# Kernel optimization log

Measured on AMD Instinct MI355X. Metric: run time of the kernel, lower is better.

Reference implementation:

```python
import jax, jax.numpy as jnp
import numpy as np

D_MODEL = 1024
N_HEADS = 16
D_HEAD = D_MODEL // N_HEADS


def setup_inputs() -> dict:
    key = jax.random.key(0)
    k1, k2, k3, k4, k5, k6 = jax.random.split(key, 6)
    B, Q, T = 4, 1024, 4096
    s = 1.0 / np.sqrt(D_MODEL)  # ~ kaiming-uniform scale for Linear weights
    return {
        "q_in": jax.random.normal(k1, (B, Q, D_MODEL), dtype=jnp.float32),
        "kv_in": jax.random.normal(k2, (B, T, D_MODEL), dtype=jnp.float32),
        "Wq": jax.random.normal(k3, (D_MODEL, D_MODEL), dtype=jnp.float32) * s,
        "Wk": jax.random.normal(k4, (D_MODEL, D_MODEL), dtype=jnp.float32) * s,
        "Wv": jax.random.normal(k5, (D_MODEL, D_MODEL), dtype=jnp.float32) * s,
        "Wo": jax.random.normal(k6, (D_MODEL, D_MODEL), dtype=jnp.float32) * s,
    }


def reference(q_in, kv_in, Wq, Wk, Wv, Wo):
    B, Q, D = q_in.shape
    T = kv_in.shape[1]
    scale = D_HEAD ** -0.5
    # projections; torch Linear: y = x @ W.T
    q = (q_in @ Wq.T).reshape(B, Q, N_HEADS, D_HEAD)
    k = (kv_in @ Wk.T).reshape(B, T, N_HEADS, D_HEAD)
    v = (kv_in @ Wv.T).reshape(B, T, N_HEADS, D_HEAD)
    # scores [B, H, Q, T]
    w = jnp.einsum("bqhd,bthd->bhqt", q, k) * scale
    w = jax.nn.softmax(w.astype(jnp.float32), axis=-1).astype(q.dtype)
    # dropout p=0.0 -> identity
    out = jnp.einsum("bhqt,bthd->bqhd", w, v).reshape(B, Q, D)
    return out @ Wo.T
```

## Files before the change

### kernel.cpp

```cpp
#include <hip/hip_runtime.h>
#include <hip/hip_bf16.h>
#include <cstdint>
#include <cstddef>

#define DM 1024
#define NH 16
#define DH 64
#define BQ 1024
#define TT 4096
#define BB 4
#define NSPLIT 2
#define TSPLIT (TT / NSPLIT)

using f32x4 = __attribute__((ext_vector_type(4))) float;
using f32x16 = __attribute__((ext_vector_type(16))) float;
using s16x8 = __attribute__((ext_vector_type(8))) short;

__device__ __forceinline__ unsigned short f2bf(float f) {
  union { __hip_bfloat16 h; unsigned short u; } c;
  c.h = __float2bfloat16(f);
  return c.u;
}

__device__ __forceinline__ float exp2_raw(float x) {
  return __builtin_amdgcn_exp2f(x);
}

__device__ __forceinline__ f32x16 fill16(float v) {
  f32x16 z;
#pragma unroll
  for (int i = 0; i < 16; i++) z[i] = v;
  return z;
}

__device__ __forceinline__ int pack2(float lo, float hi2) {
  return (int)((unsigned int)f2bf(lo) | ((unsigned int)f2bf(hi2) << 16));
}

template<int RB>
__device__ __forceinline__ s16x8 mkfrag(const f32x16& p, int hi) {
  const int W1 = pack2(p[RB + 0], p[RB + 1]);
  const int W3 = pack2(p[RB + 2], p[RB + 3]);
  const int W2 = pack2(p[RB + 4], p[RB + 5]);
  const int W4 = pack2(p[RB + 6], p[RB + 7]);
  const int s1 = __shfl_xor(W1, 32);
  const int s3 = __shfl_xor(W3, 32);
  const int s2 = __shfl_xor(W2, 32);
  const int s4 = __shfl_xor(W4, 32);
  union { int i[4]; s16x8 v; } u;
  u.i[0] = hi ? s2 : W1;
  u.i[1] = hi ? s4 : W3;
  u.i[2] = hi ? W2 : s1;
  u.i[3] = hi ? W4 : s3;
  return u.v;
}

__global__ void cvt_f32_bf16(const float* __restrict__ in, unsigned short* __restrict__ out, int n4) {
  int i = blockIdx.x * blockDim.x + threadIdx.x;
  if (i < n4) {
    float4 v = reinterpret_cast<const float4*>(in)[i];
    ushort4 o;
    o.x = f2bf(v.x); o.y = f2bf(v.y); o.z = f2bf(v.z); o.w = f2bf(v.w);
    reinterpret_cast<ushort4*>(out)[i] = o;
  }
}

__global__ void cvt_w4(const float* __restrict__ w0, const float* __restrict__ w1,
                       const float* __restrict__ w2, const float* __restrict__ w3,
                       unsigned short* __restrict__ o0, unsigned short* __restrict__ o1,
                       unsigned short* __restrict__ o2, unsigned short* __restrict__ o3,
                       int n4) {
  int i = blockIdx.x * blockDim.x + threadIdx.x;
  if (i >= n4) return;
  const float* in; unsigned short* out;
  switch (blockIdx.y) {
    case 0: in = w0; out = o0; break;
    case 1: in = w1; out = o1; break;
    case 2: in = w2; out = o2; break;
    default: in = w3; out = o3; break;
  }
  float4 v = reinterpret_cast<const float4*>(in)[i];
  ushort4 o;
  o.x = f2bf(v.x); o.y = f2bf(v.y); o.z = f2bf(v.z); o.w = f2bf(v.w);
  reinterpret_cast<ushort4*>(out)[i] = o;
}

__device__ __forceinline__ void gload_lds16(const unsigned short* g, unsigned short* l) {
  __builtin_amdgcn_global_load_lds(
      (const __attribute__((address_space(1))) unsigned int*)g,
      (__attribute__((address_space(3))) unsigned int*)l,
      16, 0, 0);
}

__device__ __forceinline__ int xcd_swz(int lin, int nwg) {
  return (lin & 7) * (nwg >> 3) + (lin >> 3);
}


#define GEMM_STAGE(AS, BS, BUF)                                              \
  do {                                                                       \
    _Pragma("unroll")                                                        \
    for (int s = 0; s < 4; s++) {                                            \
      gload_lds16(gA + (size_t)(s * 8) * DM, &AS[BUF][(wid * 32 + s * 8) * 64]); \
      gload_lds16(gW + (size_t)(s * 8) * DM, &BS[BUF][(wid * 32 + s * 8) * 64]); \
    }                                                                        \
    gA += 64; gW += 64;                                                      \
  } while (0)

#define GEMM_COMPUTE(AS, BS, BUF)                                            \
  do {                                                                       \
    __builtin_amdgcn_s_setprio(1);                                           \
    _Pragma("unroll")                                                        \
    for (int kk = 0; kk < 2; kk++) {                                         \
      s16x8 af[4], bfv[4];                                                   \
      _Pragma("unroll")                                                      \
      for (int mt = 0; mt < 4; mt++) {                                       \
        const int row = wr * 64 + mt * 16 + fr;                              \
        af[mt] = *reinterpret_cast<const s16x8*>(                            \
            &AS[BUF][row * 64 + (((kk * 4 + fkg) ^ (fr & 7)) * 8)]);         \
      }                                                                      \
      _Pragma("unroll")                                                      \
      for (int nt = 0; nt < 4; nt++) {                                       \
        const int row = wc * 64 + nt * 16 + fr;                              \
        bfv[nt] = *reinterpret_cast<const s16x8*>(                           \
            &BS[BUF][row * 64 + (((kk * 4 + fkg) ^ (fr & 7)) * 8)]);         \
      }                                                                      \
      _Pragma("unroll")                                                      \
      for (int mt = 0; mt < 4; mt++)                                         \
        _Pragma("unroll")                                                    \
        for (int nt = 0; nt < 4; nt++)                                       \
          acc[mt][nt] = __builtin_amdgcn_mfma_f32_16x16x32_bf16(             \
              af[mt], bfv[nt], acc[mt][nt], 0, 0, 0);                        \
    }                                                                        \
    __builtin_amdgcn_s_setprio(0);                                           \
  } while (0)

template<int MODE, int SEQ, bool PRESCALE, int NT>
__global__ __launch_bounds__(256) void gemm_bt(const unsigned short* __restrict__ A,
                                               const unsigned short* __restrict__ W,
                                               unsigned short* __restrict__ Cb,
                                               float* __restrict__ Cf) {
  __shared__ unsigned short As[2][128 * 64];
  __shared__ unsigned short Bs[2][128 * 64];
  const int tid = threadIdx.x;
  const int wid = tid >> 6, lane = tid & 63;
  const int swz = xcd_swz(blockIdx.x, gridDim.x);
  const int m0 = (swz / NT) * 128, n0 = (swz % NT) * 128;
  const int wr = wid >> 1, wc = wid & 1;
  const int fr = lane & 15;
  const int fkg = lane >> 4;

  f32x4 acc[4][4];
#pragma unroll
  for (int mt = 0; mt < 4; mt++)
#pragma unroll
    for (int nt = 0; nt < 4; nt++) acc[mt][nt] = f32x4{0.f, 0.f, 0.f, 0.f};

  const int srow = lane >> 3;
  const int sc8 = (lane & 7) ^ (srow & 7);
  const unsigned short* gA = A + (size_t)(m0 + wid * 32 + srow) * DM + sc8 * 8;
  const unsigned short* gW = W + (size_t)(n0 + wid * 32 + srow) * DM + sc8 * 8;

  GEMM_STAGE(As, Bs, 0);
  __syncthreads();
  for (int kt = 0; kt < DM / 64; kt += 2) {
    if (kt + 1 < DM / 64) GEMM_STAGE(As, Bs, 1);
    GEMM_COMPUTE(As, Bs, 0);
    __syncthreads();
    if (kt + 2 < DM / 64) GEMM_STAGE(As, Bs, 0);
    GEMM_COMPUTE(As, Bs, 1);
    __syncthreads();
  }

#pragma unroll
  for (int mt = 0; mt < 4; mt++) {
#pragma unroll
    for (int nt = 0; nt < 4; nt++) {
      const int col = n0 + wc * 64 + nt * 16 + fr;
#pragma unroll
      for (int r = 0; r < 4; r++) {
        const int m = m0 + wr * 64 + mt * 16 + (lane >> 4) * 4 + r;
        float v = acc[mt][nt][r];
        if constexpr (PRESCALE) v *= 0.18033688011112042f;
        if constexpr (MODE == 0) {
          const int b = m / SEQ, sr = m % SEQ;
          const int h = col >> 6, dh = col & 63;
          Cb[((size_t)(b * NH + h) * SEQ + sr) * DH + dh] = f2bf(v);
        } else {
          Cf[(size_t)m * DM + col] = v;
        }
      }
    }
  }
}

__global__ __launch_bounds__(256) void gemm_kv(const unsigned short* __restrict__ A,
                                               const unsigned short* __restrict__ Wkv,
                                               unsigned short* __restrict__ Kp,
                                               unsigned short* __restrict__ Vt) {
  __shared__ unsigned short As[2][128 * 64];
  __shared__ unsigned short Bs[2][128 * 64];
  const int tid = threadIdx.x;
  const int wid = tid >> 6, lane = tid & 63;
  const int swz = xcd_swz(blockIdx.x, gridDim.x);
  const int m0 = (swz >> 4) * 128, n0 = (swz & 15) * 128;
  const int wr = wid >> 1, wc = wid & 1;
  const int fr = lane & 15;
  const int fkg = lane >> 4;

  f32x4 acc[4][4];
#pragma unroll
  for (int mt = 0; mt < 4; mt++)
#pragma unroll
    for (int nt = 0; nt < 4; nt++) acc[mt][nt] = f32x4{0.f, 0.f, 0.f, 0.f};

  const int srow = lane >> 3;
  const int sc8 = (lane & 7) ^ (srow & 7);
  const unsigned short* gA = A + (size_t)(m0 + wid * 32 + srow) * DM + sc8 * 8;
  const unsigned short* gW = Wkv + (size_t)(n0 + wid * 32 + srow) * DM + sc8 * 8;

  GEMM_STAGE(As, Bs, 0);
  __syncthreads();
  for (int kt = 0; kt < DM / 64; kt += 2) {
    if (kt + 1 < DM / 64) GEMM_STAGE(As, Bs, 1);
    GEMM_COMPUTE(As, Bs, 0);
    __syncthreads();
    if (kt + 2 < DM / 64) GEMM_STAGE(As, Bs, 0);
    GEMM_COMPUTE(As, Bs, 1);
    __syncthreads();
  }

  const int klg = lane >> 4;
#pragma unroll
  for (int mt = 0; mt < 4; mt++) {
#pragma unroll
    for (int nt = 0; nt < 4; nt++) {
      const int col = n0 + wc * 64 + nt * 16 + fr;
      const int tb = m0 + wr * 64 + mt * 16 + klg * 4;
      const int b = tb >> 12, sr = tb & (TT - 1);
      if (col < DM) {
        const int h = col >> 6, dh = col & 63;
#pragma unroll
        for (int r = 0; r < 4; r++)
          Kp[((size_t)(b * NH + h) * TT + sr + r) * DH + dh] = f2bf(acc[mt][nt][r]);
      } else {
        const int c2 = col - DM;
        const int h = c2 >> 6, dh = c2 & 63;
        ushort4 pk;
        pk.x = f2bf(acc[mt][nt][0]);
        pk.y = f2bf(acc[mt][nt][1]);
        pk.z = f2bf(acc[mt][nt][2]);
        pk.w = f2bf(acc[mt][nt][3]);
        *reinterpret_cast<ushort4*>(&Vt[((size_t)(b * NH + h) * DH + dh) * TT + sr]) = pk;
      }
    }
  }
}

#define ATTN_TILE(CUR, DO_STAGE, SBUF)                                             \
  do {                                                                             \
    if (DO_STAGE) {                                                                \
      gload_lds16(gK, &KVs[(SBUF)][wid * 512]);                                    \
      gload_lds16(gV, &KVs[2 + (SBUF)][wid * 512]);                                \
      gK += 64 * DH; gV += 64;                                                     \
    }                                                                              \
    f32x16 s0 = fill16(-7.0f), s1 = fill16(-7.0f);                                 \
    __builtin_amdgcn_s_setprio(1);                                                 \
    _Pragma("unroll")                                                              \
    for (int kk = 0; kk < 4; kk++) {                                               \
      s16x8 kb0 = *reinterpret_cast<const s16x8*>(lds0 + (CUR) * 8192 + offA[kk]); \
      s0 = __builtin_amdgcn_mfma_f32_32x32x16_bf16(kb0, qf[kk], s0, 0, 0, 0);      \
      s16x8 kb1 = *reinterpret_cast<const s16x8*>(lds0 + (CUR) * 8192 + offB[kk]); \
      s1 = __builtin_amdgcn_mfma_f32_32x32x16_bf16(kb1, qf[kk], s1, 0, 0, 0);      \
    }                                                                              \
    __builtin_amdgcn_s_setprio(0);                                                 \
    _Pragma("unroll")                                                              \
    for (int r = 0; r < 16; r++) {                                                 \
      s0[r] = exp2_raw(s0[r]); lsum += s0[r];                                      \
      s1[r] = exp2_raw(s1[r]); lsum += s1[r];                                      \
    }                                                                              \
    s16x8 pa[4];                                                                   \
    pa[0] = mkfrag<0>(s0, hi);                                                     \
    pa[1] = mkfrag<8>(s0, hi);                                                     \
    pa[2] = mkfrag<0>(s1, hi);                                                     \
    pa[3] = mkfrag<8>(s1, hi);                                                     \
    __builtin_amdgcn_s_setprio(1);                                                 \
    _Pragma("unroll")                                                              \
    for (int kk = 0; kk < 4; kk++) {                                               \
      s16x8 vb0 = *reinterpret_cast<const s16x8*>(lds0 + 16384 + (CUR) * 8192 + offA[kk]); \
      o0 = __builtin_amdgcn_mfma_f32_32x32x16_bf16(pa[kk], vb0, o0, 0, 0, 0);      \
      s16x8 vb1 = *reinterpret_cast<const s16x8*>(lds0 + 16384 + (CUR) * 8192 + offB[kk]); \
      o1 = __builtin_amdgcn_mfma_f32_32x32x16_bf16(pa[kk], vb1, o1, 0, 0, 0);      \
    }                                                                              \
    __builtin_amdgcn_s_setprio(0);                                                 \
    __syncthreads();                                                               \
  } while (0)

__global__ __launch_bounds__(512, 4) void attn_kern(const unsigned short* __restrict__ Qp,
                                                    const unsigned short* __restrict__ Kp,
                                                    const unsigned short* __restrict__ Vtg,
                                                    float* __restrict__ Opart,
                                                    float* __restrict__ lsums) {
  __shared__ unsigned short KVs[4][64 * 64];
  const int bh = blockIdx.x;
  const int q0 = blockIdx.y * 256;
  const int split = blockIdx.z;
  const int t00 = split * TSPLIT;
  const int tid = threadIdx.x, wid = tid >> 6, lane = tid & 63;
  const int l31 = lane & 31, hi = lane >> 5;

  const size_t qrow = (size_t)bh * BQ + q0 + wid * 32 + l31;
  s16x8 qf[4];
#pragma unroll
  for (int kk = 0; kk < 4; kk++)
    qf[kk] = *reinterpret_cast<const s16x8*>(&Qp[qrow * DH + 16 * kk + 8 * hi]);

  f32x16 o0 = fill16(0.f), o1 = fill16(0.f);
  float lsum = 0.f;

  const size_t kvbase = (size_t)bh * TT * DH;
  const int rk = tid >> 3;
  const int c8 = tid & 7;

  const unsigned short* gK = Kp + kvbase + (size_t)(t00 + rk) * DH + (c8 ^ (rk & 7)) * 8;
  const unsigned short* gV = Vtg + kvbase + (size_t)rk * TT + t00 + (c8 ^ (rk & 7)) * 8;

  const char* lds0 = (const char*)&KVs[0][0];
  const int sw = l31 & 7;
  int offA[4], offB[4];
#pragma unroll
  for (int kk = 0; kk < 4; kk++) {
    offA[kk] = (l31 * 64 + (((2 * kk + hi) ^ sw) * 8)) * 2;
    offB[kk] = ((32 + l31) * 64 + (((2 * kk + hi) ^ sw) * 8)) * 2;
  }

  gload_lds16(gK, &KVs[0][wid * 512]);
  gload_lds16(gV, &KVs[2][wid * 512]);
  gK += 64 * DH; gV += 64;
  __syncthreads();

  const int NIT = TSPLIT / 128;
  for (int it2 = 0; it2 < NIT; ++it2) {
    ATTN_TILE(0, true, 1);
    ATTN_TILE(1, (it2 < NIT - 1), 0);
  }

  lsum += __shfl_xor(lsum, 32);
  if (lane < 32)
    lsums[((size_t)split * (BB * NH) + bh) * BQ + q0 + wid * 32 + lane] = lsum;

#pragma unroll
  for (int r = 0; r < 16; r++) {
    const int q = (r & 3) + 8 * (r >> 2) + 4 * hi;
    const size_t orow = (((size_t)split * (BB * NH) + bh) * BQ + q0 + wid * 32 + q) * DH;
    Opart[orow + l31] = o0[r];
    Opart[orow + 32 + l31] = o1[r];
  }
}

__global__ __launch_bounds__(256) void attn_combine(const float* __restrict__ Opart,
                                                    const float* __restrict__ lsums,
                                                    unsigned short* __restrict__ Ob) {
  const int gid = blockIdx.x * 256 + threadIdx.x;
  const int row = gid >> 4, seg = gid & 15;
  float denom = 0.f;
#pragma unroll
  for (int s = 0; s < NSPLIT; s++) denom += lsums[(size_t)s * (BB * NH * BQ) + row];
  const float inv = 1.0f / denom;
  float4 acc = {0.f, 0.f, 0.f, 0.f};
#pragma unroll
  for (int s = 0; s < NSPLIT; s++) {
    const float4 p = reinterpret_cast<const float4*>(Opart)[(size_t)s * (BB * NH * BQ) * 16 + (size_t)row * 16 + seg];
    acc.x += p.x; acc.y += p.y; acc.z += p.z; acc.w += p.w;
  }
  const int bh = row >> 10, q = row & (BQ - 1);
  const int b = bh >> 4, h = bh & 15;
  ushort4 o;
  o.x = f2bf(acc.x * inv);
  o.y = f2bf(acc.y * inv);
  o.z = f2bf(acc.z * inv);
  o.w = f2bf(acc.w * inv);
  *reinterpret_cast<ushort4*>(&Ob[((size_t)b * BQ + q) * DM + h * DH + seg * 4]) = o;
}

extern "C" void kernel_launch(void* const* d_in, const int* in_sizes, int n_in,
                              void* d_out, int out_size, void* d_ws, size_t ws_size,
                              hipStream_t stream) {
  const float* q_in = (const float*)d_in[0];
  const float* kv_in = (const float*)d_in[1];
  const float* Wq = (const float*)d_in[2];
  const float* Wk = (const float*)d_in[3];
  const float* Wv = (const float*)d_in[4];
  const float* Wo = (const float*)d_in[5];
  float* out = (float*)d_out;

  char* ws = (char*)d_ws;
  unsigned short* qin_b = (unsigned short*)ws;  ws += (size_t)BB * BQ * DM * 2;
  unsigned short* kvin_b = (unsigned short*)ws; ws += (size_t)BB * TT * DM * 2;
  unsigned short* Wq_b = (unsigned short*)ws;   ws += (size_t)DM * DM * 2;
  unsigned short* Wk_b = (unsigned short*)ws;   ws += (size_t)DM * DM * 2;
  unsigned short* Wv_b = (unsigned short*)ws;   ws += (size_t)DM * DM * 2;
  unsigned short* Wo_b = (unsigned short*)ws;   ws += (size_t)DM * DM * 2;
  unsigned short* qp = (unsigned short*)ws;     ws += (size_t)BB * NH * BQ * DH * 2;
  unsigned short* kp = (unsigned short*)ws;     ws += (size_t)BB * NH * TT * DH * 2;
  unsigned short* vt = (unsigned short*)ws;     ws += (size_t)BB * NH * DH * TT * 2;
  unsigned short* ao = (unsigned short*)ws;     ws += (size_t)BB * BQ * DM * 2;
  float* Opart = (float*)ws;                    ws += (size_t)NSPLIT * BB * NH * BQ * DH * 4;
  float* lsums = (float*)ws;                    ws += (size_t)NSPLIT * BB * NH * BQ * 4;

  const int qn4 = BB * BQ * DM / 4;
  const int kvn4 = BB * TT * DM / 4;
  const int wn4 = DM * DM / 4;
  cvt_f32_bf16<<<(qn4 + 255) / 256, 256, 0, stream>>>(q_in, qin_b, qn4);
  cvt_f32_bf16<<<(kvn4 + 255) / 256, 256, 0, stream>>>(kv_in, kvin_b, kvn4);
  cvt_w4<<<dim3((wn4 + 255) / 256, 4), 256, 0, stream>>>(Wq, Wk, Wv, Wo,
                                                         Wq_b, Wk_b, Wv_b, Wo_b, wn4);

  dim3 blk(256);
  gemm_bt<0, BQ, true, 8><<<dim3(BB * BQ / 128 * 8), blk, 0, stream>>>(qin_b, Wq_b, qp, nullptr);
  gemm_kv<<<dim3(BB * TT / 128 * 16), blk, 0, stream>>>(kvin_b, Wk_b, kp, vt);

  attn_kern<<<dim3(BB * NH, BQ / 256, NSPLIT), dim3(512), 0, stream>>>(qp, kp, vt, Opart, lsums);
  attn_combine<<<dim3(BB * NH * BQ * 16 / 256), blk, 0, stream>>>(Opart, lsums, ao);

  gemm_bt<1, BQ, false, 8><<<dim3(BB * BQ / 128 * 8), blk, 0, stream>>>(ao, Wo_b, nullptr, out);
}
```

Baseline: 243.7 us.

## Merge conversion and projection launches, double KV tile depth in attention

Merges the three fp32-to-bf16 conversion kernels into one launch, and merges the Q and KV projection GEMMs into one launch of 2304 blocks that branch on block index. The attention kernel now stages two 64-row K/V tiles per buffer slot (LDS doubled to 8 slots) and syncs once per 128 keys instead of once per 64. This cuts launch count, tail effects and barrier overhead. The cost is larger LDS use per block, which may lower attention occupancy.

```diff
diff --git a/kernel.cpp b/kernel.cpp
--- a/kernel.cpp
+++ b/kernel.cpp
@@ -55,34 +55,41 @@
   return u.v;
 }
 
-__global__ void cvt_f32_bf16(const float* __restrict__ in, unsigned short* __restrict__ out, int n4) {
+__global__ void cvt_all(const float* __restrict__ q_in, const float* __restrict__ kv_in,
+                        const float* __restrict__ w0, const float* __restrict__ w1,
+                        const float* __restrict__ w2, const float* __restrict__ w3,
+                        unsigned short* __restrict__ qo, unsigned short* __restrict__ kvo,
+                        unsigned short* __restrict__ o0, unsigned short* __restrict__ o1,
+                        unsigned short* __restrict__ o2, unsigned short* __restrict__ o3) {
+  const int KVN4 = BB * TT * DM / 4;
+  const int QN4 = BB * BQ * DM / 4;
+  const int WN4 = DM * DM / 4;
   int i = blockIdx.x * blockDim.x + threadIdx.x;
-  if (i < n4) {
-    float4 v = reinterpret_cast<const float4*>(in)[i];
-    ushort4 o;
-    o.x = f2bf(v.x); o.y = f2bf(v.y); o.z = f2bf(v.z); o.w = f2bf(v.w);
-    reinterpret_cast<ushort4*>(out)[i] = o;
-  }
-}
-
-__global__ void cvt_w4(const float* __restrict__ w0, const float* __restrict__ w1,
-                       const float* __restrict__ w2, const float* __restrict__ w3,
-                       unsigned short* __restrict__ o0, unsigned short* __restrict__ o1,
-                       unsigned short* __restrict__ o2, unsigned short* __restrict__ o3,
-                       int n4) {
-  int i = blockIdx.x * blockDim.x + threadIdx.x;
-  if (i >= n4) return;
-  const float* in; unsigned short* out;
-  switch (blockIdx.y) {
-    case 0: in = w0; out = o0; break;
-    case 1: in = w1; out = o1; break;
-    case 2: in = w2; out = o2; break;
-    default: in = w3; out = o3; break;
-  }
-  float4 v = reinterpret_cast<const float4*>(in)[i];
+  const float* in;
+  unsigned short* out;
+  int idx;
+  if (i < KVN4) {
+    in = kv_in; out = kvo; idx = i;
+  } else {
+    i -= KVN4;
+    if (i < QN4) {
+      in = q_in; out = qo; idx = i;
+    } else {
+      i -= QN4;
+      const int t = i >> 18;
+      idx = i & (WN4 - 1);
+      switch (t) {
+        case 0: in = w0; out = o0; break;
+        case 1: in = w1; out = o1; break;
+        case 2: in = w2; out = o2; break;
+        default: in = w3; out = o3; break;
+      }
+    }
+  }
+  float4 v = reinterpret_cast<const float4*>(in)[idx];
   ushort4 o;
   o.x = f2bf(v.x); o.y = f2bf(v.y); o.z = f2bf(v.z); o.w = f2bf(v.w);
-  reinterpret_cast<ushort4*>(out)[i] = o;
+  reinterpret_cast<ushort4*>(out)[idx] = o;
 }
 
 __device__ __forceinline__ void gload_lds16(const unsigned short* g, unsigned short* l) {
@@ -135,10 +142,103 @@
     __builtin_amdgcn_s_setprio(0);                                           \
   } while (0)
 
-template<int MODE, int SEQ, bool PRESCALE, int NT>
+__global__ __launch_bounds__(256) void gemm_proj(const unsigned short* __restrict__ qA,
+                                                 const unsigned short* __restrict__ kvA,
+                                                 const unsigned short* __restrict__ Wqb,
+                                                 const unsigned short* __restrict__ Wkv,
+                                                 unsigned short* __restrict__ Qp,
+                                                 unsigned short* __restrict__ Kp,
+                                                 unsigned short* __restrict__ Vt) {
+  __shared__ unsigned short As[2][128 * 64];
+  __shared__ unsigned short Bs[2][128 * 64];
+  const int tid = threadIdx.x;
+  const int wid = tid >> 6, lane = tid & 63;
+  const int swz = xcd_swz(blockIdx.x, gridDim.x);
+  const bool isQ = swz >= 2048;
+  int m0, n0;
+  const unsigned short *Abase, *Wbase;
+  if (isQ) {
+    const int qi = swz - 2048;
+    m0 = (qi >> 3) * 128; n0 = (qi & 7) * 128;
+    Abase = qA; Wbase = Wqb;
+  } else {
+    m0 = (swz >> 4) * 128; n0 = (swz & 15) * 128;
+    Abase = kvA; Wbase = Wkv;
+  }
+  const int wr = wid >> 1, wc = wid & 1;
+  const int fr = lane & 15;
+  const int fkg = lane >> 4;
+
+  f32x4 acc[4][4];
+#pragma unroll
+  for (int mt = 0; mt < 4; mt++)
+#pragma unroll
+    for (int nt = 0; nt < 4; nt++) acc[mt][nt] = f32x4{0.f, 0.f, 0.f, 0.f};
+
+  const int srow = lane >> 3;
+  const int sc8 = (lane & 7) ^ (srow & 7);
+  const unsigned short* gA = Abase + (size_t)(m0 + wid * 32 + srow) * DM + sc8 * 8;
+  const unsigned short* gW = Wbase + (size_t)(n0 + wid * 32 + srow) * DM + sc8 * 8;
+
+  GEMM_STAGE(As, Bs, 0);
+  __syncthreads();
+  for (int kt = 0; kt < DM / 64; kt += 2) {
+    if (kt + 1 < DM / 64) GEMM_STAGE(As, Bs, 1);
+    GEMM_COMPUTE(As, Bs, 0);
+    __syncthreads();
+    if (kt + 2 < DM / 64) GEMM_STAGE(As, Bs, 0);
+    GEMM_COMPUTE(As, Bs, 1);
+    __syncthreads();
+  }
+
+  const int klg = lane >> 4;
+  if (isQ) {
+#pragma unroll
+    for (int mt = 0; mt < 4; mt++) {
+#pragma unroll
+      for (int nt = 0; nt < 4; nt++) {
+        const int col = n0 + wc * 64 + nt * 16 + fr;
+        const int h = col >> 6, dh = col & 63;
+#pragma unroll
+        for (int r = 0; r < 4; r++) {
+          const int m = m0 + wr * 64 + mt * 16 + klg * 4 + r;
+          const int b = m >> 10, sr = m & (BQ - 1);
+          Qp[((size_t)(b * NH + h) * BQ + sr) * DH + dh] =
+              f2bf(acc[mt][nt][r] * 0.18033688011112042f);
+        }
+      }
+    }
+  } else {
+#pragma unroll
+    for (int mt = 0; mt < 4; mt++) {
+#pragma unroll
+      for (int nt = 0; nt < 4; nt++) {
+        const int col = n0 + wc * 64 + nt * 16 + fr;
+        const int tb = m0 + wr * 64 + mt * 16 + klg * 4;
+        const int b = tb >> 12, sr = tb & (TT - 1);
+        if (col < DM) {
+          const int h = col >> 6, dh = col & 63;
+#pragma unroll
+          for (int r = 0; r < 4; r++)
+            Kp[((size_t)(b * NH + h) * TT + sr + r) * DH + dh] = f2bf(acc[mt][nt][r]);
+        } else {
+          const int c2 = col - DM;
+          const int h = c2 >> 6, dh = c2 & 63;
+          ushort4 pk;
+          pk.x = f2bf(acc[mt][nt][0]);
+          pk.y = f2bf(acc[mt][nt][1]);
+          pk.z = f2bf(acc[mt][nt][2]);
+          pk.w = f2bf(acc[mt][nt][3]);
+          *reinterpret_cast<ushort4*>(&Vt[((size_t)(b * NH + h) * DH + dh) * TT + sr]) = pk;
+        }
+      }
+    }
+  }
+}
+
+template<int NT>
 __global__ __launch_bounds__(256) void gemm_bt(const unsigned short* __restrict__ A,
                                                const unsigned short* __restrict__ W,
-                                               unsigned short* __restrict__ Cb,
                                                float* __restrict__ Cf) {
   __shared__ unsigned short As[2][128 * 64];
   __shared__ unsigned short Bs[2][128 * 64];
@@ -180,97 +280,31 @@
 #pragma unroll
       for (int r = 0; r < 4; r++) {
         const int m = m0 + wr * 64 + mt * 16 + (lane >> 4) * 4 + r;
-        float v = acc[mt][nt][r];
-        if constexpr (PRESCALE) v *= 0.18033688011112042f;
-        if constexpr (MODE == 0) {
-          const int b = m / SEQ, sr = m % SEQ;
-          const int h = col >> 6, dh = col & 63;
-          Cb[((size_t)(b * NH + h) * SEQ + sr) * DH + dh] = f2bf(v);
-        } else {
-          Cf[(size_t)m * DM + col] = v;
-        }
+        Cf[(size_t)m * DM + col] = acc[mt][nt][r];
       }
     }
   }
 }
 
-__global__ __launch_bounds__(256) void gemm_kv(const unsigned short* __restrict__ A,
-                                               const unsigned short* __restrict__ Wkv,
-                                               unsigned short* __restrict__ Kp,
-                                               unsigned short* __restrict__ Vt) {
-  __shared__ unsigned short As[2][128 * 64];
-  __shared__ unsigned short Bs[2][128 * 64];
-  const int tid = threadIdx.x;
-  const int wid = tid >> 6, lane = tid & 63;
-  const int swz = xcd_swz(blockIdx.x, gridDim.x);
-  const int m0 = (swz >> 4) * 128, n0 = (swz & 15) * 128;
-  const int wr = wid >> 1, wc = wid & 1;
-  const int fr = lane & 15;
-  const int fkg = lane >> 4;
-
-  f32x4 acc[4][4];
-#pragma unroll
-  for (int mt = 0; mt < 4; mt++)
-#pragma unroll
-    for (int nt = 0; nt < 4; nt++) acc[mt][nt] = f32x4{0.f, 0.f, 0.f, 0.f};
-
-  const int srow = lane >> 3;
-  const int sc8 = (lane & 7) ^ (srow & 7);
-  const unsigned short* gA = A + (size_t)(m0 + wid * 32 + srow) * DM + sc8 * 8;
-  const unsigned short* gW = Wkv + (size_t)(n0 + wid * 32 + srow) * DM + sc8 * 8;
-
-  GEMM_STAGE(As, Bs, 0);
-  __syncthreads();
-  for (int kt = 0; kt < DM / 64; kt += 2) {
-    if (kt + 1 < DM / 64) GEMM_STAGE(As, Bs, 1);
-    GEMM_COMPUTE(As, Bs, 0);
-    __syncthreads();
-    if (kt + 2 < DM / 64) GEMM_STAGE(As, Bs, 0);
-    GEMM_COMPUTE(As, Bs, 1);
-    __syncthreads();
-  }
-
-  const int klg = lane >> 4;
-#pragma unroll
-  for (int mt = 0; mt < 4; mt++) {
-#pragma unroll
-    for (int nt = 0; nt < 4; nt++) {
-      const int col = n0 + wc * 64 + nt * 16 + fr;
-      const int tb = m0 + wr * 64 + mt * 16 + klg * 4;
-      const int b = tb >> 12, sr = tb & (TT - 1);
-      if (col < DM) {
-        const int h = col >> 6, dh = col & 63;
-#pragma unroll
-        for (int r = 0; r < 4; r++)
-          Kp[((size_t)(b * NH + h) * TT + sr + r) * DH + dh] = f2bf(acc[mt][nt][r]);
-      } else {
-        const int c2 = col - DM;
-        const int h = c2 >> 6, dh = c2 & 63;
-        ushort4 pk;
-        pk.x = f2bf(acc[mt][nt][0]);
-        pk.y = f2bf(acc[mt][nt][1]);
-        pk.z = f2bf(acc[mt][nt][2]);
-        pk.w = f2bf(acc[mt][nt][3]);
-        *reinterpret_cast<ushort4*>(&Vt[((size_t)(b * NH + h) * DH + dh) * TT + sr]) = pk;
-      }
-    }
-  }
-}
-
-#define ATTN_TILE(CUR, DO_STAGE, SBUF)                                             \
+
+#define ATTN_STAGE(SP)                                                       \
+  do {                                                                       \
+    gload_lds16(gK, &KVs[(SP) * 2][wid * 512]);                              \
+    gload_lds16(gK + 64 * DH, &KVs[(SP) * 2 + 1][wid * 512]);                \
+    gload_lds16(gV, &KVs[4 + (SP) * 2][wid * 512]);                          \
+    gload_lds16(gV + 64, &KVs[4 + (SP) * 2 + 1][wid * 512]);                 \
+    gK += 128 * DH; gV += 128;                                               \
+  } while (0)
+
+#define ATTN_COMPUTE(SLOT)                                                         \
   do {                                                                             \
-    if (DO_STAGE) {                                                                \
-      gload_lds16(gK, &KVs[(SBUF)][wid * 512]);                                    \
-      gload_lds16(gV, &KVs[2 + (SBUF)][wid * 512]);                                \
-      gK += 64 * DH; gV += 64;                                                     \
-    }                                                                              \
     f32x16 s0 = fill16(-7.0f), s1 = fill16(-7.0f);                                 \
     __builtin_amdgcn_s_setprio(1);                                                 \
     _Pragma("unroll")                                                              \
     for (int kk = 0; kk < 4; kk++) {                                               \
-      s16x8 kb0 = *reinterpret_cast<const s16x8*>(lds0 + (CUR) * 8192 + offA[kk]); \
+      s16x8 kb0 = *reinterpret_cast<const s16x8*>(lds0 + (SLOT) * 8192 + offA[kk]); \
       s0 = __builtin_amdgcn_mfma_f32_32x32x16_bf16(kb0, qf[kk], s0, 0, 0, 0);      \
-      s16x8 kb1 = *reinterpret_cast<const s16x8*>(lds0 + (CUR) * 8192 + offB[kk]); \
+      s16x8 kb1 = *reinterpret_cast<const s16x8*>(lds0 + (SLOT) * 8192 + offB[kk]); \
       s1 = __builtin_amdgcn_mfma_f32_32x32x16_bf16(kb1, qf[kk], s1, 0, 0, 0);      \
     }                                                                              \
     __builtin_amdgcn_s_setprio(0);                                                 \
@@ -287,13 +321,12 @@
     __builtin_amdgcn_s_setprio(1);                                                 \
     _Pragma("unroll")                                                              \
     for (int kk = 0; kk < 4; kk++) {                                               \
-      s16x8 vb0 = *reinterpret_cast<const s16x8*>(lds0 + 16384 + (CUR) * 8192 + offA[kk]); \
+      s16x8 vb0 = *reinterpret_cast<const s16x8*>(lds0 + 32768 + (SLOT) * 8192 + offA[kk]); \
       o0 = __builtin_amdgcn_mfma_f32_32x32x16_bf16(pa[kk], vb0, o0, 0, 0, 0);      \
-      s16x8 vb1 = *reinterpret_cast<const s16x8*>(lds0 + 16384 + (CUR) * 8192 + offB[kk]); \
+      s16x8 vb1 = *reinterpret_cast<const s16x8*>(lds0 + 32768 + (SLOT) * 8192 + offB[kk]); \
       o1 = __builtin_amdgcn_mfma_f32_32x32x16_bf16(pa[kk], vb1, o1, 0, 0, 0);      \
     }                                                                              \
     __builtin_amdgcn_s_setprio(0);                                                 \
-    __syncthreads();                                                               \
   } while (0)
 
 __global__ __launch_bounds__(512, 4) void attn_kern(const unsigned short* __restrict__ Qp,
@@ -301,7 +334,7 @@
                                                     const unsigned short* __restrict__ Vtg,
                                                     float* __restrict__ Opart,
                                                     float* __restrict__ lsums) {
-  __shared__ unsigned short KVs[4][64 * 64];
+  __shared__ unsigned short KVs[8][64 * 64];
   const int bh = blockIdx.x;
   const int q0 = blockIdx.y * 256;
   const int split = blockIdx.z;
@@ -334,15 +367,19 @@
     offB[kk] = ((32 + l31) * 64 + (((2 * kk + hi) ^ sw) * 8)) * 2;
   }
 
-  gload_lds16(gK, &KVs[0][wid * 512]);
-  gload_lds16(gV, &KVs[2][wid * 512]);
-  gK += 64 * DH; gV += 64;
+  ATTN_STAGE(0);
   __syncthreads();
 
-  const int NIT = TSPLIT / 128;
-  for (int it2 = 0; it2 < NIT; ++it2) {
-    ATTN_TILE(0, true, 1);
-    ATTN_TILE(1, (it2 < NIT - 1), 0);
+  const int NSETS = TSPLIT / 128;
+  for (int it2 = 0; it2 < NSETS / 2; ++it2) {
+    if (2 * it2 + 1 < NSETS) ATTN_STAGE(1);
+    ATTN_COMPUTE(0);
+    ATTN_COMPUTE(1);
+    __syncthreads();
+    if (2 * it2 + 2 < NSETS) ATTN_STAGE(0);
+    ATTN_COMPUTE(2);
+    ATTN_COMPUTE(3);
+    __syncthreads();
   }
 
   lsum += __shfl_xor(lsum, 32);
@@ -408,20 +445,15 @@
   float* Opart = (float*)ws;                    ws += (size_t)NSPLIT * BB * NH * BQ * DH * 4;
   float* lsums = (float*)ws;                    ws += (size_t)NSPLIT * BB * NH * BQ * 4;
 
-  const int qn4 = BB * BQ * DM / 4;
-  const int kvn4 = BB * TT * DM / 4;
-  const int wn4 = DM * DM / 4;
-  cvt_f32_bf16<<<(qn4 + 255) / 256, 256, 0, stream>>>(q_in, qin_b, qn4);
-  cvt_f32_bf16<<<(kvn4 + 255) / 256, 256, 0, stream>>>(kv_in, kvin_b, kvn4);
-  cvt_w4<<<dim3((wn4 + 255) / 256, 4), 256, 0, stream>>>(Wq, Wk, Wv, Wo,
-                                                         Wq_b, Wk_b, Wv_b, Wo_b, wn4);
+  const int totn4 = (BB * TT * DM + BB * BQ * DM + 4 * DM * DM) / 4;
+  cvt_all<<<dim3(totn4 / 256), dim3(256), 0, stream>>>(q_in, kv_in, Wq, Wk, Wv, Wo,
+                                                       qin_b, kvin_b, Wq_b, Wk_b, Wv_b, Wo_b);
 
   dim3 blk(256);
-  gemm_bt<0, BQ, true, 8><<<dim3(BB * BQ / 128 * 8), blk, 0, stream>>>(qin_b, Wq_b, qp, nullptr);
-  gemm_kv<<<dim3(BB * TT / 128 * 16), blk, 0, stream>>>(kvin_b, Wk_b, kp, vt);
+  gemm_proj<<<dim3(2304), blk, 0, stream>>>(qin_b, kvin_b, Wq_b, Wk_b, qp, kp, vt);
 
   attn_kern<<<dim3(BB * NH, BQ / 256, NSPLIT), dim3(512), 0, stream>>>(qp, kp, vt, Opart, lsums);
   attn_combine<<<dim3(BB * NH * BQ * 16 / 256), blk, 0, stream>>>(Opart, lsums, ao);
 
-  gemm_bt<1, BQ, false, 8><<<dim3(BB * BQ / 128 * 8), blk, 0, stream>>>(ao, Wo_b, nullptr, out);
-}
+  gemm_bt<8><<<dim3(BB * BQ / 128 * 8), blk, 0, stream>>>(ao, Wo_b, out);
+}
```

New measurement: 498.7 us. 105% more time.
